# Kernel optimization log

Hardware: AMD Instinct MI355X
Metric: run time of the kernel (lower is better)

Reference implementation:

```python
import jax, jax.numpy as jnp
import numpy as np
import math

D_MODEL = 768
N_HEADS = 12
HEAD_DIM = D_MODEL // N_HEADS


def setup_inputs() -> dict:
    key = jax.random.key(0)
    ks = jax.random.split(key, 9)
    B, S = 2, 4096
    scale = 1.0 / math.sqrt(D_MODEL)
    x = jax.random.normal(ks[0], (B, S, D_MODEL), dtype=jnp.float32)
    # Linear weights stored as [in, out] for x @ W; biases [out].
    Wq = jax.random.normal(ks[1], (D_MODEL, D_MODEL), dtype=jnp.float32) * scale
    bq = jax.random.normal(ks[2], (D_MODEL,), dtype=jnp.float32) * 0.01
    Wk = jax.random.normal(ks[3], (D_MODEL, D_MODEL), dtype=jnp.float32) * scale
    bk = jax.random.normal(ks[4], (D_MODEL,), dtype=jnp.float32) * 0.01
    Wv = jax.random.normal(ks[5], (D_MODEL, D_MODEL), dtype=jnp.float32) * scale
    bv = jax.random.normal(ks[6], (D_MODEL,), dtype=jnp.float32) * 0.01
    Wo = jax.random.normal(ks[7], (D_MODEL, D_MODEL), dtype=jnp.float32) * scale
    bo = jax.random.normal(ks[8], (D_MODEL,), dtype=jnp.float32) * 0.01
    return {"x": x, "Wq": Wq, "bq": bq, "Wk": Wk, "bk": bk,
            "Wv": Wv, "bv": bv, "Wo": Wo, "bo": bo}


def reference(x, Wq, bq, Wk, bk, Wv, bv, Wo, bo):
    B, S, _ = x.shape
    def split_heads(t):  # [B,S,D] -> [B,H,S,hd]
        return t.reshape(B, S, N_HEADS, HEAD_DIM).transpose(0, 2, 1, 3)
    Q = split_heads(x @ Wq + bq)
    K = split_heads(x @ Wk + bk)
    V = split_heads(x @ Wv + bv)
    scores = jnp.einsum('bhqd,bhkd->bhqk', Q, K) / math.sqrt(HEAD_DIM)
    attn = jax.nn.softmax(scores, axis=-1)
    ctx = jnp.einsum('bhqk,bhkd->bhqd', attn, V)  # [B,H,S,hd]
    ctx = ctx.transpose(0, 2, 1, 3).reshape(B, S, D_MODEL)
    return ctx @ Wo + bo
```

## Files before the change

kernel.cpp:

```cpp
#include <hip/hip_runtime.h>

typedef __bf16 bf16x8 __attribute__((ext_vector_type(8)));
typedef float f32x4 __attribute__((ext_vector_type(4)));
typedef float f32x16 __attribute__((ext_vector_type(16)));
typedef unsigned short u16x8 __attribute__((ext_vector_type(8)));

#define DEV static __device__ __forceinline__

DEV unsigned short f2bf(float f) {
  unsigned u = __builtin_bit_cast(unsigned, f);
  u += 0x7fffu + ((u >> 16) & 1u);
  return (unsigned short)(u >> 16);
}
DEV unsigned cvt_pk_bf16(float lo, float hi) {
  unsigned r;
  asm("v_cvt_pk_bf16_f32 %0, %1, %2" : "=v"(r) : "v"(lo), "v"(hi));
  return r;
}
DEV float exp2_fast(float x) {
  float r;
  asm("v_exp_f32 %0, %1" : "=v"(r) : "v"(x));
  return r;
}
DEV void gload16(const void* g, void* lds) {
  __builtin_amdgcn_global_load_lds(
      (__attribute__((address_space(1))) void*)(g),
      (__attribute__((address_space(3))) void*)(lds), 16, 0, 0);
}

__global__ __launch_bounds__(256) void k_cvt_x(const float* __restrict__ x,
                                               unsigned short* __restrict__ xb) {
  const int i = (blockIdx.x * 256 + threadIdx.x) * 4;
  float4 v = *(const float4*)(x + i);
  ushort4 o;
  o.x = f2bf(v.x); o.y = f2bf(v.y); o.z = f2bf(v.z); o.w = f2bf(v.w);
  *(ushort4*)(xb + i) = o;
}

__global__ __launch_bounds__(256) void k_tw(const float* __restrict__ Wq, const float* __restrict__ Wk,
                                            const float* __restrict__ Wv, const float* __restrict__ Wo,
                                            unsigned short* __restrict__ Wt, unsigned short* __restrict__ Wot) {
  __shared__ float tile[32][33];
  const int z = blockIdx.z;
  const float* W = (z == 0) ? Wq : (z == 1) ? Wk : (z == 2) ? Wv : Wo;
  const int n0 = blockIdx.x * 32, k0 = blockIdx.y * 32;
  const int tx = threadIdx.x, ty = threadIdx.y;
#pragma unroll
  for (int j = 0; j < 4; j++)
    tile[ty + 8 * j][tx] = W[(size_t)(k0 + ty + 8 * j) * 768 + n0 + tx];
  __syncthreads();
  unsigned short* dst = (z == 3) ? Wot : (Wt + (size_t)z * 768 * 768);
#pragma unroll
  for (int j = 0; j < 4; j++)
    dst[(size_t)(n0 + ty + 8 * j) * 768 + k0 + tx] = f2bf(tile[tx][ty + 8 * j]);
}

template <bool F32OUT>
__global__ __launch_bounds__(256, 2) void k_gemm(
    const unsigned short* __restrict__ A, const unsigned short* __restrict__ Bt,
    const float* __restrict__ b0, const float* __restrict__ b1, const float* __restrict__ b2,
    void* __restrict__ out, int M, int K) {
  __shared__ char As[8192];
  __shared__ char Bs[8192];
  const int t = threadIdx.x;
  const int l = t & 63, w = t >> 6;
  const int lr = l & 15, lg = l >> 4;
  const int m0 = blockIdx.y * 128, n0 = blockIdx.x * 128;
  const int wr = (w >> 1) * 64, wc = (w & 1) * 64;

  f32x4 acc[4][4];
#pragma unroll
  for (int i = 0; i < 4; i++)
#pragma unroll
    for (int j = 0; j < 4; j++)
#pragma unroll
      for (int r = 0; r < 4; r++) acc[i][j][r] = 0.0f;

  const int rA0 = t >> 2, rA1 = 64 + (t >> 2);
  const int cbl = (t & 3) * 16;
  const int cb0 = cbl ^ ((rA0 & 3) << 4);
  const int cb1 = cbl ^ ((rA1 & 3) << 4);
  const size_t K2 = (size_t)K * 2;
  const char* ga0 = (const char*)A + (size_t)(m0 + rA0) * K2 + cb0;
  const char* ga1 = (const char*)A + (size_t)(m0 + rA1) * K2 + cb1;
  const char* gb0 = (const char*)Bt + (size_t)(n0 + rA0) * K2 + cb0;
  const char* gb1 = (const char*)Bt + (size_t)(n0 + rA1) * K2 + cb1;
  char* AsW = As + w * 1024;
  char* BsW = Bs + w * 1024;

  const int nkt = K >> 5;
  for (int kt = 0; kt < nkt; ++kt) {
    const size_t ko = (size_t)kt * 64;
    gload16(ga0 + ko, AsW);
    gload16(ga1 + ko, AsW + 4096);
    gload16(gb0 + ko, BsW);
    gload16(gb1 + ko, BsW + 4096);
    __syncthreads();
    bf16x8 af[4], bfr[4];
#pragma unroll
    for (int mi = 0; mi < 4; mi++) {
      const int row = wr + mi * 16 + lr;
      af[mi] = *(const bf16x8*)(As + row * 64 + ((lg * 16) ^ ((row & 3) << 4)));
    }
#pragma unroll
    for (int ni = 0; ni < 4; ni++) {
      const int row = wc + ni * 16 + lr;
      bfr[ni] = *(const bf16x8*)(Bs + row * 64 + ((lg * 16) ^ ((row & 3) << 4)));
    }
#pragma unroll
    for (int mi = 0; mi < 4; mi++)
#pragma unroll
      for (int ni = 0; ni < 4; ni++)
        acc[mi][ni] = __builtin_amdgcn_mfma_f32_16x16x32_bf16(af[mi], bfr[ni], acc[mi][ni], 0, 0, 0);
    __syncthreads();
  }

  if constexpr (F32OUT) {
    float* o = (float*)out;
#pragma unroll
    for (int mi = 0; mi < 4; mi++)
#pragma unroll
      for (int ni = 0; ni < 4; ni++) {
        const int col = n0 + wc + ni * 16 + lr;
        const int rowb = m0 + wr + mi * 16 + lg * 4;
        const float bias = b0[col];
#pragma unroll
        for (int r = 0; r < 4; r++)
          o[(size_t)(rowb + r) * 768 + col] = acc[mi][ni][r] + bias;
      }
  } else {
    const int sel = n0 / 768;
    const int cbase = n0 - sel * 768;
    const float* bp = (sel == 0) ? b0 : ((sel == 1) ? b1 : b2);
    unsigned short* o = (unsigned short*)out + (size_t)sel * M * 768;
#pragma unroll
    for (int mi = 0; mi < 4; mi++)
#pragma unroll
      for (int ni = 0; ni < 4; ni++) {
        const int ci = cbase + wc + ni * 16 + lr;
        const int rowb = m0 + wr + mi * 16 + lg * 4;
        const float bias = bp[ci];
#pragma unroll
        for (int r = 0; r < 4; r++)
          o[(size_t)(rowb + r) * 768 + ci] = f2bf(acc[mi][ni][r] + bias);
      }
  }
}

__global__ __launch_bounds__(256) void k_tv(const unsigned short* __restrict__ V,
                                            unsigned short* __restrict__ Vt) {
  __shared__ unsigned short tile[64][68];
  const int t = threadIdx.x;
  const int s0 = blockIdx.x * 64;
  const int h = blockIdx.y;
  const int b = blockIdx.z;
#pragma unroll
  for (int j = 0; j < 4; j++) {
    const int c = j * 256 + t;
    const int r = c >> 4, cc = c & 15;
    *(ushort4*)(&tile[r][cc * 4]) =
        *(const ushort4*)(V + (size_t)(b * 4096 + s0 + r) * 768 + h * 64 + cc * 4);
  }
  __syncthreads();
#pragma unroll
  for (int j = 0; j < 2; j++) {
    const int c = j * 256 + t;
    const int d = c >> 3, sc = c & 7;
    u16x8 vv;
#pragma unroll
    for (int e = 0; e < 8; e++) vv[e] = tile[sc * 8 + e][d];
    *(u16x8*)(Vt + (size_t)((b * 12 + h) * 64 + d) * 4096 + s0 + sc * 8) = vv;
  }
}

__global__ __launch_bounds__(256, 2) void k_attn(
    const unsigned short* __restrict__ Q, const unsigned short* __restrict__ Kg,
    const unsigned short* __restrict__ Vt, unsigned short* __restrict__ Ctx) {
  __shared__ char Ks[8192];
  __shared__ char Vs[8192];
  __shared__ char Ps[16384];
  const int t = threadIdx.x;
  const int l = t & 63, w = t >> 6;
  const int lq = l & 31, hi = l >> 5;
  const int bh = blockIdx.y, b = bh / 12, h = bh % 12;
  const int q0 = blockIdx.x * 128 + w * 32;

  bf16x8 qf[4];
  {
    const char* qrow = (const char*)Q + ((size_t)(b * 4096 + q0 + lq) * 768 + h * 64) * 2;
#pragma unroll
    for (int kst = 0; kst < 4; kst++)
      qf[kst] = *(const bf16x8*)(qrow + kst * 32 + hi * 16);
  }

  f32x16 cacc[2];
#pragma unroll
  for (int d = 0; d < 2; d++)
#pragma unroll
    for (int r = 0; r < 16; r++) cacc[d][r] = 0.0f;
  float m_run = -1e30f, l_run = 0.0f;

  const int rS0 = t >> 3, rS1 = 32 + (t >> 3);
  const int cblS = (t & 7) * 16;
  const int cbS0 = cblS ^ ((rS0 & 7) << 4);
  const int cbS1 = cblS ^ ((rS1 & 7) << 4);
  char* KsW = Ks + w * 1024;
  char* VsW = Vs + w * 1024;
  char* Pw = Ps + w * 4096;
  const char* Kbase = (const char*)Kg + ((size_t)(b * 4096) * 768 + h * 64) * 2;
  const char* Vbase = (const char*)Vt + (size_t)(bh * 64) * 4096 * 2;

  const float C = 0.18033688011112042f;
  const int swq = (lq & 7) << 4;

  for (int kv0 = 0; kv0 < 4096; kv0 += 64) {
    gload16(Kbase + (size_t)(kv0 + rS0) * 1536 + cbS0, KsW);
    gload16(Kbase + (size_t)(kv0 + rS1) * 1536 + cbS1, KsW + 4096);
    gload16(Vbase + (size_t)rS0 * 8192 + kv0 * 2 + cbS0, VsW);
    gload16(Vbase + (size_t)rS1 * 8192 + kv0 * 2 + cbS1, VsW + 4096);
    __syncthreads();

    f32x16 st[2];
#pragma unroll
    for (int nt = 0; nt < 2; nt++) {
#pragma unroll
      for (int r = 0; r < 16; r++) st[nt][r] = 0.0f;
      const int row = nt * 32 + lq;
      const int sw = (row & 7) << 4;
#pragma unroll
      for (int kst = 0; kst < 4; kst++) {
        bf16x8 kf = *(const bf16x8*)(Ks + row * 128 + ((kst * 32 + hi * 16) ^ sw));
        st[nt] = __builtin_amdgcn_mfma_f32_32x32x16_bf16(kf, qf[kst], st[nt], 0, 0, 0);
      }
    }

    float tmax = -1e30f;
#pragma unroll
    for (int nt = 0; nt < 2; nt++)
#pragma unroll
      for (int r = 0; r < 16; r++) {
        st[nt][r] *= C;
        tmax = fmaxf(tmax, st[nt][r]);
      }
    tmax = fmaxf(tmax, __shfl_xor(tmax, 32));
    const float m_new = fmaxf(m_run, tmax);
    const float alpha = exp2_fast(m_run - m_new);
    float tsum = 0.0f;
#pragma unroll
    for (int nt = 0; nt < 2; nt++)
#pragma unroll
      for (int r = 0; r < 16; r++) {
        const float p = exp2_fast(st[nt][r] - m_new);
        st[nt][r] = p;
        tsum += p;
      }
    tsum += __shfl_xor(tsum, 32);
    l_run = l_run * alpha + tsum;
    m_run = m_new;
#pragma unroll
    for (int d = 0; d < 2; d++)
#pragma unroll
      for (int r = 0; r < 16; r++) cacc[d][r] *= alpha;

#pragma unroll
    for (int nt = 0; nt < 2; nt++)
#pragma unroll
      for (int p4 = 0; p4 < 4; p4++) {
        const unsigned u0 = cvt_pk_bf16(st[nt][p4 * 4 + 0], st[nt][p4 * 4 + 1]);
        const unsigned u1 = cvt_pk_bf16(st[nt][p4 * 4 + 2], st[nt][p4 * 4 + 3]);
        const int cbp = nt * 64 + p4 * 16 + hi * 8;
        uint2 uu; uu.x = u0; uu.y = u1;
        *(uint2*)(Pw + lq * 128 + ((cbp ^ swq))) = uu;
      }

#pragma unroll
    for (int kst = 0; kst < 4; kst++) {
      bf16x8 pb = *(const bf16x8*)(Pw + lq * 128 + ((kst * 32 + hi * 16) ^ swq));
#pragma unroll
      for (int ntd = 0; ntd < 2; ntd++) {
        const int row = ntd * 32 + lq;
        bf16x8 av = *(const bf16x8*)(Vs + row * 128 + ((kst * 32 + hi * 16) ^ ((row & 7) << 4)));
        cacc[ntd] = __builtin_amdgcn_mfma_f32_32x32x16_bf16(av, pb, cacc[ntd], 0, 0, 0);
      }
    }
    __syncthreads();
  }

  const float inv_l = 1.0f / l_run;
#pragma unroll
  for (int ntd = 0; ntd < 2; ntd++)
#pragma unroll
    for (int p4 = 0; p4 < 4; p4++) {
      const unsigned u0 = cvt_pk_bf16(cacc[ntd][p4 * 4 + 0] * inv_l, cacc[ntd][p4 * 4 + 1] * inv_l);
      const unsigned u1 = cvt_pk_bf16(cacc[ntd][p4 * 4 + 2] * inv_l, cacc[ntd][p4 * 4 + 3] * inv_l);
      const int cbp = ntd * 64 + p4 * 16 + hi * 8;
      uint2 uu; uu.x = u0; uu.y = u1;
      *(uint2*)(Pw + lq * 128 + cbp) = uu;
    }
#pragma unroll
  for (int j = 0; j < 4; j++) {
    const int c = j * 64 + l;
    const int qq = c >> 3, c8 = c & 7;
    u16x8 v = *(const u16x8*)(Pw + qq * 128 + c8 * 16);
    *(u16x8*)((char*)Ctx + ((size_t)(b * 4096 + q0 + qq) * 768 + h * 64 + c8 * 8) * 2) = v;
  }
}

extern "C" void kernel_launch(void* const* d_in, const int* in_sizes, int n_in,
                              void* d_out, int out_size, void* d_ws, size_t ws_size,
                              hipStream_t stream) {
  const float* x  = (const float*)d_in[0];
  const float* Wq = (const float*)d_in[1];
  const float* bq = (const float*)d_in[2];
  const float* Wk = (const float*)d_in[3];
  const float* bk = (const float*)d_in[4];
  const float* Wv = (const float*)d_in[5];
  const float* bv = (const float*)d_in[6];
  const float* Wo = (const float*)d_in[7];
  const float* bo = (const float*)d_in[8];

  char* ws = (char*)d_ws;
  unsigned short* Xb  = (unsigned short*)(ws);
  unsigned short* Wt  = (unsigned short*)(ws + 12582912);
  unsigned short* Wot = (unsigned short*)(ws + 16121856);
  unsigned short* QKV = (unsigned short*)(ws + 17301504);
  unsigned short* Vtr = (unsigned short*)(ws + 55050240);
  unsigned short* Ctx = (unsigned short*)(ws + 67633152);
  unsigned short* Qp = QKV;
  unsigned short* Kp = QKV + (size_t)8192 * 768;
  unsigned short* Vp = QKV + (size_t)2 * 8192 * 768;

  k_cvt_x<<<6144, 256, 0, stream>>>(x, Xb);
  k_tw<<<dim3(24, 24, 4), dim3(32, 8), 0, stream>>>(Wq, Wk, Wv, Wo, Wt, Wot);
  k_gemm<false><<<dim3(18, 64), 256, 0, stream>>>(Xb, Wt, bq, bk, bv, (void*)QKV, 8192, 768);
  k_tv<<<dim3(64, 12, 2), 256, 0, stream>>>(Vp, Vtr);
  k_attn<<<dim3(32, 24), 256, 0, stream>>>(Qp, Kp, Vtr, Ctx);
  k_gemm<true><<<dim3(6, 64), 256, 0, stream>>>(Ctx, Wot, bo, bo, bo, d_out, 8192, 768);
}
```

Before: 317.6 us.

## Double-buffer attention K/V, keep P in registers, lazy rescale, fold Q scale

The attention kernel now double-buffers the K/V LDS tiles so global-to-LDS loads for the next tile overlap compute on the current one. The probability matrix is passed to the PV MFMA through permlane32 swaps instead of a round trip through LDS. Online-softmax rescaling is skipped unless the max grows by more than a threshold, and the softmax scale is folded into the Q projection epilogue. It also adds s_setprio around MFMA sections, precomputes LDS offsets and swaps grid axes so heads vary fastest, which risks register pressure and relies on the reduced-rescale numerics staying bounded.

```diff
diff --git a/kernel.cpp b/kernel.cpp
--- a/kernel.cpp
+++ b/kernel.cpp
@@ -4,6 +4,7 @@
 typedef float f32x4 __attribute__((ext_vector_type(4)));
 typedef float f32x16 __attribute__((ext_vector_type(16)));
 typedef unsigned short u16x8 __attribute__((ext_vector_type(8)));
+typedef unsigned int u32x4 __attribute__((ext_vector_type(4)));
 
 #define DEV static __device__ __forceinline__
 
@@ -21,6 +22,11 @@
   float r;
   asm("v_exp_f32 %0, %1" : "=v"(r) : "v"(x));
   return r;
+}
+DEV void plswap(unsigned& a, unsigned& b) {
+  auto r = __builtin_amdgcn_permlane32_swap(a, b, false, false);
+  a = r[0];
+  b = r[1];
 }
 DEV void gload16(const void* g, void* lds) {
   __builtin_amdgcn_global_load_lds(
@@ -59,7 +65,7 @@
 __global__ __launch_bounds__(256, 2) void k_gemm(
     const unsigned short* __restrict__ A, const unsigned short* __restrict__ Bt,
     const float* __restrict__ b0, const float* __restrict__ b1, const float* __restrict__ b2,
-    void* __restrict__ out, int M, int K) {
+    void* __restrict__ out, int M, int K, float scale0) {
   __shared__ char As[8192];
   __shared__ char Bs[8192];
   const int t = threadIdx.x;
@@ -132,6 +138,7 @@
     const int sel = n0 / 768;
     const int cbase = n0 - sel * 768;
     const float* bp = (sel == 0) ? b0 : ((sel == 1) ? b1 : b2);
+    const float sc = (sel == 0) ? scale0 : 1.0f;
     unsigned short* o = (unsigned short*)out + (size_t)sel * M * 768;
 #pragma unroll
     for (int mi = 0; mi < 4; mi++)
@@ -142,7 +149,7 @@
         const float bias = bp[ci];
 #pragma unroll
         for (int r = 0; r < 4; r++)
-          o[(size_t)(rowb + r) * 768 + ci] = f2bf(acc[mi][ni][r] + bias);
+          o[(size_t)(rowb + r) * 768 + ci] = f2bf((acc[mi][ni][r] + bias) * sc);
       }
   }
 }
@@ -176,14 +183,13 @@
 __global__ __launch_bounds__(256, 2) void k_attn(
     const unsigned short* __restrict__ Q, const unsigned short* __restrict__ Kg,
     const unsigned short* __restrict__ Vt, unsigned short* __restrict__ Ctx) {
-  __shared__ char Ks[8192];
-  __shared__ char Vs[8192];
-  __shared__ char Ps[16384];
+  __shared__ char Kd[2][8192];
+  __shared__ char Vd[2][8192];
   const int t = threadIdx.x;
   const int l = t & 63, w = t >> 6;
   const int lq = l & 31, hi = l >> 5;
-  const int bh = blockIdx.y, b = bh / 12, h = bh % 12;
-  const int q0 = blockIdx.x * 128 + w * 32;
+  const int bh = blockIdx.x, b = bh / 12, h = bh % 12;
+  const int q0 = blockIdx.y * 128 + w * 32;
 
   bf16x8 qf[4];
   {
@@ -199,93 +205,111 @@
 #pragma unroll
     for (int r = 0; r < 16; r++) cacc[d][r] = 0.0f;
   float m_run = -1e30f, l_run = 0.0f;
+
+  unsigned koff[2][4];
+#pragma unroll
+  for (int nt = 0; nt < 2; nt++)
+#pragma unroll
+    for (int kst = 0; kst < 4; kst++)
+      koff[nt][kst] = (unsigned)((nt * 32 + lq) * 128 + ((kst * 32 + hi * 16) ^ ((lq & 7) << 4)));
 
   const int rS0 = t >> 3, rS1 = 32 + (t >> 3);
   const int cblS = (t & 7) * 16;
   const int cbS0 = cblS ^ ((rS0 & 7) << 4);
   const int cbS1 = cblS ^ ((rS1 & 7) << 4);
-  char* KsW = Ks + w * 1024;
-  char* VsW = Vs + w * 1024;
-  char* Pw = Ps + w * 4096;
-  const char* Kbase = (const char*)Kg + ((size_t)(b * 4096) * 768 + h * 64) * 2;
-  const char* Vbase = (const char*)Vt + (size_t)(bh * 64) * 4096 * 2;
-
-  const float C = 0.18033688011112042f;
-  const int swq = (lq & 7) << 4;
-
-  for (int kv0 = 0; kv0 < 4096; kv0 += 64) {
-    gload16(Kbase + (size_t)(kv0 + rS0) * 1536 + cbS0, KsW);
-    gload16(Kbase + (size_t)(kv0 + rS1) * 1536 + cbS1, KsW + 4096);
-    gload16(Vbase + (size_t)rS0 * 8192 + kv0 * 2 + cbS0, VsW);
-    gload16(Vbase + (size_t)rS1 * 8192 + kv0 * 2 + cbS1, VsW + 4096);
-    __syncthreads();
-
+  const char* gK0 = (const char*)Kg + ((size_t)(b * 4096 + rS0) * 768 + h * 64) * 2 + cbS0;
+  const char* gK1 = (const char*)Kg + ((size_t)(b * 4096 + rS1) * 768 + h * 64) * 2 + cbS1;
+  const char* gV0 = (const char*)Vt + ((size_t)(bh * 64 + rS0) * 4096) * 2 + cbS0;
+  const char* gV1 = (const char*)Vt + ((size_t)(bh * 64 + rS1) * 4096) * 2 + cbS1;
+  char* KdW0 = Kd[0] + w * 1024;
+  char* VdW0 = Vd[0] + w * 1024;
+
+  auto STAGE = [&](int buf) {
+    gload16(gK0, KdW0 + buf * 8192);
+    gload16(gK1, KdW0 + buf * 8192 + 4096);
+    gload16(gV0, VdW0 + buf * 8192);
+    gload16(gV1, VdW0 + buf * 8192 + 4096);
+    gK0 += 98304; gK1 += 98304;
+    gV0 += 128;   gV1 += 128;
+  };
+
+  auto COMPUTE = [&](const char* Kb, const char* Vb) {
     f32x16 st[2];
+    __builtin_amdgcn_s_setprio(1);
 #pragma unroll
     for (int nt = 0; nt < 2; nt++) {
 #pragma unroll
       for (int r = 0; r < 16; r++) st[nt][r] = 0.0f;
-      const int row = nt * 32 + lq;
-      const int sw = (row & 7) << 4;
 #pragma unroll
       for (int kst = 0; kst < 4; kst++) {
-        bf16x8 kf = *(const bf16x8*)(Ks + row * 128 + ((kst * 32 + hi * 16) ^ sw));
+        bf16x8 kf = *(const bf16x8*)(Kb + koff[nt][kst]);
         st[nt] = __builtin_amdgcn_mfma_f32_32x32x16_bf16(kf, qf[kst], st[nt], 0, 0, 0);
       }
     }
+    __builtin_amdgcn_s_setprio(0);
 
     float tmax = -1e30f;
 #pragma unroll
     for (int nt = 0; nt < 2; nt++)
 #pragma unroll
+      for (int r = 0; r < 16; r++) tmax = fmaxf(tmax, st[nt][r]);
+    tmax = fmaxf(tmax, __shfl_xor(tmax, 32));
+    if (__any(tmax > m_run + 8.0f)) {
+      const float m_new = fmaxf(m_run, tmax);
+      const float alpha = exp2_fast(m_run - m_new);
+      l_run *= alpha;
+#pragma unroll
+      for (int d = 0; d < 2; d++)
+#pragma unroll
+        for (int r = 0; r < 16; r++) cacc[d][r] *= alpha;
+      m_run = m_new;
+    }
+    float tsum = 0.0f;
+#pragma unroll
+    for (int nt = 0; nt < 2; nt++)
+#pragma unroll
       for (int r = 0; r < 16; r++) {
-        st[nt][r] *= C;
-        tmax = fmaxf(tmax, st[nt][r]);
-      }
-    tmax = fmaxf(tmax, __shfl_xor(tmax, 32));
-    const float m_new = fmaxf(m_run, tmax);
-    const float alpha = exp2_fast(m_run - m_new);
-    float tsum = 0.0f;
-#pragma unroll
-    for (int nt = 0; nt < 2; nt++)
-#pragma unroll
-      for (int r = 0; r < 16; r++) {
-        const float p = exp2_fast(st[nt][r] - m_new);
+        const float p = exp2_fast(st[nt][r] - m_run);
         st[nt][r] = p;
         tsum += p;
       }
     tsum += __shfl_xor(tsum, 32);
-    l_run = l_run * alpha + tsum;
-    m_run = m_new;
-#pragma unroll
-    for (int d = 0; d < 2; d++)
-#pragma unroll
-      for (int r = 0; r < 16; r++) cacc[d][r] *= alpha;
-
-#pragma unroll
-    for (int nt = 0; nt < 2; nt++)
-#pragma unroll
-      for (int p4 = 0; p4 < 4; p4++) {
-        const unsigned u0 = cvt_pk_bf16(st[nt][p4 * 4 + 0], st[nt][p4 * 4 + 1]);
-        const unsigned u1 = cvt_pk_bf16(st[nt][p4 * 4 + 2], st[nt][p4 * 4 + 3]);
-        const int cbp = nt * 64 + p4 * 16 + hi * 8;
-        uint2 uu; uu.x = u0; uu.y = u1;
-        *(uint2*)(Pw + lq * 128 + ((cbp ^ swq))) = uu;
-      }
-
+    l_run += tsum;
+
+    __builtin_amdgcn_s_setprio(1);
 #pragma unroll
     for (int kst = 0; kst < 4; kst++) {
-      bf16x8 pb = *(const bf16x8*)(Pw + lq * 128 + ((kst * 32 + hi * 16) ^ swq));
+      const f32x16& P = st[kst >> 1];
+      const int r0 = (kst & 1) * 8;
+      unsigned A0 = cvt_pk_bf16(P[r0 + 0], P[r0 + 1]);
+      unsigned A1 = cvt_pk_bf16(P[r0 + 2], P[r0 + 3]);
+      unsigned B0 = cvt_pk_bf16(P[r0 + 4], P[r0 + 5]);
+      unsigned B1 = cvt_pk_bf16(P[r0 + 6], P[r0 + 7]);
+      plswap(A0, B0);
+      plswap(A1, B1);
+      u32x4 pw; pw[0] = A0; pw[1] = A1; pw[2] = B0; pw[3] = B1;
+      const bf16x8 pb = __builtin_bit_cast(bf16x8, pw);
 #pragma unroll
       for (int ntd = 0; ntd < 2; ntd++) {
-        const int row = ntd * 32 + lq;
-        bf16x8 av = *(const bf16x8*)(Vs + row * 128 + ((kst * 32 + hi * 16) ^ ((row & 7) << 4)));
+        bf16x8 av = *(const bf16x8*)(Vb + koff[ntd][kst]);
         cacc[ntd] = __builtin_amdgcn_mfma_f32_32x32x16_bf16(av, pb, cacc[ntd], 0, 0, 0);
       }
     }
+    __builtin_amdgcn_s_setprio(0);
+  };
+
+  STAGE(0);
+  __syncthreads();
+  for (int kvt = 0; kvt < 64; kvt += 2) {
+    STAGE(1);
+    COMPUTE(Kd[0], Vd[0]);
     __syncthreads();
-  }
-
+    if (kvt + 2 < 64) STAGE(0);
+    COMPUTE(Kd[1], Vd[1]);
+    __syncthreads();
+  }
+
+  char* scratch = Kd[0] + w * 4096;
   const float inv_l = 1.0f / l_run;
 #pragma unroll
   for (int ntd = 0; ntd < 2; ntd++)
@@ -293,15 +317,14 @@
     for (int p4 = 0; p4 < 4; p4++) {
       const unsigned u0 = cvt_pk_bf16(cacc[ntd][p4 * 4 + 0] * inv_l, cacc[ntd][p4 * 4 + 1] * inv_l);
       const unsigned u1 = cvt_pk_bf16(cacc[ntd][p4 * 4 + 2] * inv_l, cacc[ntd][p4 * 4 + 3] * inv_l);
-      const int cbp = ntd * 64 + p4 * 16 + hi * 8;
       uint2 uu; uu.x = u0; uu.y = u1;
-      *(uint2*)(Pw + lq * 128 + cbp) = uu;
+      *(uint2*)(scratch + lq * 128 + ntd * 64 + p4 * 16 + hi * 8) = uu;
     }
 #pragma unroll
   for (int j = 0; j < 4; j++) {
     const int c = j * 64 + l;
     const int qq = c >> 3, c8 = c & 7;
-    u16x8 v = *(const u16x8*)(Pw + qq * 128 + c8 * 16);
+    u16x8 v = *(const u16x8*)(scratch + qq * 128 + c8 * 16);
     *(u16x8*)((char*)Ctx + ((size_t)(b * 4096 + q0 + qq) * 768 + h * 64 + c8 * 8) * 2) = v;
   }
 }
@@ -330,10 +353,12 @@
   unsigned short* Kp = QKV + (size_t)8192 * 768;
   unsigned short* Vp = QKV + (size_t)2 * 8192 * 768;
 
+  const float qscale = 0.18033688011112042f;
+
   k_cvt_x<<<6144, 256, 0, stream>>>(x, Xb);
   k_tw<<<dim3(24, 24, 4), dim3(32, 8), 0, stream>>>(Wq, Wk, Wv, Wo, Wt, Wot);
-  k_gemm<false><<<dim3(18, 64), 256, 0, stream>>>(Xb, Wt, bq, bk, bv, (void*)QKV, 8192, 768);
+  k_gemm<false><<<dim3(18, 64), 256, 0, stream>>>(Xb, Wt, bq, bk, bv, (void*)QKV, 8192, 768, qscale);
   k_tv<<<dim3(64, 12, 2), 256, 0, stream>>>(Vp, Vtr);
-  k_attn<<<dim3(32, 24), 256, 0, stream>>>(Qp, Kp, Vtr, Ctx);
-  k_gemm<true><<<dim3(6, 64), 256, 0, stream>>>(Ctx, Wot, bo, bo, bo, d_out, 8192, 768);
-}
+  k_attn<<<dim3(24, 32), 256, 0, stream>>>(Qp, Kp, Vtr, Ctx);
+  k_gemm<true><<<dim3(6, 64), 256, 0, stream>>>(Ctx, Wot, bo, bo, bo, d_out, 8192, 768, 1.0f);
+}
```

After: 294.3 us. -7.4%, faster.
